# Performance work log

Hardware: AMD Instinct MI355X
Metric: run time of the kernel (lower is better)

The kernel has to match this reference:

```python
import jax, jax.numpy as jnp
import numpy as np

H = 8          # n_heads
DK = 128       # d_model // h
D = H * DK     # d_model = 1024
B, S = 8, 1024
D_LIST = (32, 64, 96, 128)  # sorted set of hidden//h from config dict


def setup_inputs() -> dict:
    key = jax.random.key(0)
    ks = jax.random.split(key, 13)
    mk = lambda k, shape: jax.random.normal(k, shape, dtype=jnp.float32)
    inp = {
        'query': mk(ks[0], (B, S, D)),
        'key': mk(ks[1], (B, S, D)),
        'value': mk(ks[2], (B, S, D)),
        'config_idx': jax.random.randint(ks[3], (B,), 0, len(D_LIST), dtype=jnp.int32),
        'Wq': mk(ks[4], (D, D)) * 0.02, 'bq': jnp.zeros((D,), jnp.float32),
        'Wk': mk(ks[5], (D, D)) * 0.02, 'bk': jnp.zeros((D,), jnp.float32),
        'Wv': mk(ks[6], (D, D)) * 0.02, 'bv': jnp.zeros((D,), jnp.float32),
        'Wo': mk(ks[7], (D, D)) * 0.02, 'bo': jnp.zeros((D,), jnp.float32),
    }
    return inp


def _mha_arrange(query, key, value, config_idx, Wq, bq, Wk, bk, Wv, bv, Wo, bo):
    Bb, Ss, _ = query.shape
    proj = lambda x, W, b: (x @ W.T + b).reshape(Bb, Ss, H, DK).transpose(0, 2, 1, 3)
    q = proj(query, Wq, bq)   # [B,H,S,DK]
    k = proj(key, Wk, bk)
    v = proj(value, Wv, bv)
    scores = jnp.einsum('bhqd,bhkd->bhqk', q, k) / np.float32(np.sqrt(DK))
    p = jax.nn.softmax(scores, axis=-1)
    ctx = jnp.einsum('bhqk,bhkd->bhqd', p, v).transpose(0, 2, 1, 3)  # [B,S,H,DK]
    # attn_arrange: per-sample width d; pack first d dims of each head densely
    ret = jnp.zeros((Bb, Ss, H * DK), query.dtype)
    for i, d in enumerate(D_LIST):
        packed = ctx[:, :, :, :d].reshape(Bb, Ss, H * d)           # [B,S,H*d]
        packed = jnp.pad(packed, ((0, 0), (0, 0), (0, H * (DK - d))))
        sel = (config_idx == i)[:, None, None]
        ret = ret + jnp.where(sel, packed, jnp.zeros((), query.dtype))
    return ret @ Wo.T + bo


def reference(query, key, value, config_idx, Wq, bq, Wk, bk, Wv, bv, Wo, bo):
    return _mha_arrange(query, key, value, config_idx, Wq, bq, Wk, bk, Wv, bv, Wo, bo)
```

## Files before the change

kernel.cpp:

```cpp
#include <hip/hip_runtime.h>
#include <hip/hip_bf16.h>


typedef __attribute__((ext_vector_type(8))) __bf16 bf16x8;
typedef __attribute__((ext_vector_type(4))) float f32x4;

#define DEV static __device__ __forceinline__

DEV float exp2v(float x) { return __builtin_amdgcn_exp2f(x); }

DEV unsigned short f2bf(float f) {
  union { float f; unsigned int u; } c; c.f = f;
  unsigned int u = c.u + 0x7fffu + ((c.u >> 16) & 1u);
  return (unsigned short)(u >> 16);
}

DEV unsigned cvtpk(float a, float b) {
  unsigned r;
  asm("v_cvt_pk_bf16_f32 %0, %1, %2" : "=v"(r) : "v"(a), "v"(b));
  return r;
}

DEV void gload16(const void* g, void* l) {
  __builtin_amdgcn_global_load_lds((const __attribute__((address_space(1))) void*)g,
                                   (__attribute__((address_space(3))) void*)l, 16, 0, 0);
}

#define LGKM0 do { asm volatile("s_waitcnt lgkmcnt(0)" ::: "memory"); \
                   __builtin_amdgcn_sched_barrier(0); } while (0)
#define BAR   __builtin_amdgcn_s_barrier()
#define VMC4  asm volatile("s_waitcnt vmcnt(4)" ::: "memory")
#define VMC0  asm volatile("s_waitcnt vmcnt(0)" ::: "memory")

DEV void cv4(const float* __restrict__ s, unsigned short* __restrict__ d, int i) {
  const float4 a = *(const float4*)(s + i);
  ushort4 o;
  o.x = f2bf(a.x); o.y = f2bf(a.y); o.z = f2bf(a.z); o.w = f2bf(a.w);
  *(ushort4*)(d + i) = o;
}

__global__ __launch_bounds__(256) void convert_kernel(
    const float* __restrict__ q, const float* __restrict__ k, const float* __restrict__ v,
    const float* __restrict__ wq, const float* __restrict__ wk,
    const float* __restrict__ wv, const float* __restrict__ wo,
    unsigned short* __restrict__ xq, unsigned short* __restrict__ xk,
    unsigned short* __restrict__ xv, unsigned short* __restrict__ wb)
{
  const int i = (blockIdx.x * 256 + threadIdx.x) * 4;
  cv4(q, xq, i);
  cv4(k, xk, i);
  cv4(v, xv, i);
  if (i < 4 * 1024 * 1024) {
    const int which = i >> 20, off = i & 1048575;
    const float* s = which == 0 ? wq : which == 1 ? wk : which == 2 ? wv : wo;
    cv4(s, wb + (which << 20), off);
  }
}

template<int OUTMODE>
__global__ __launch_bounds__(512, 2) void gemm8p(
    const unsigned short* __restrict__ xq, const unsigned short* __restrict__ xk,
    const unsigned short* __restrict__ xv, const unsigned short* __restrict__ wb,
    const float* __restrict__ bq, const float* __restrict__ bk,
    const float* __restrict__ bv,
    unsigned short* __restrict__ Qp, unsigned short* __restrict__ Kp,
    unsigned short* __restrict__ VTp, float* __restrict__ fout)
{
  __shared__ __align__(16) char LDS[131072];
  int z, mt, nt;
  if (OUTMODE == 0) {
    const int swz = ((blockIdx.x & 7) * 48) + (blockIdx.x >> 3);
    z = swz >> 7; const int rem = swz & 127; mt = rem >> 2; nt = rem & 3;
  } else {
    const int swz = ((blockIdx.x & 7) * 16) + (blockIdx.x >> 3);
    z = 0; mt = swz >> 2; nt = swz & 3;
  }
  const int m0 = mt * 256, n0 = nt * 256;
  const unsigned short* Ag = (OUTMODE == 1) ? xq : (z == 0 ? xq : z == 1 ? xk : xv);
  const unsigned short* Bg = (OUTMODE == 1) ? wb : wb + ((size_t)z << 20);
  const float* bias = (OUTMODE == 1) ? bq : (z == 0 ? bq : z == 1 ? bk : bv);

  const int tid = threadIdx.x, lane = tid & 63, w = tid >> 6;
  const int wm = w >> 2, wn = w & 3;
  const int g = lane >> 4, ln = lane & 15;

  const f32x4 fzero = {0.f, 0.f, 0.f, 0.f};
  f32x4 acc[8][4];
#pragma unroll
  for (int i = 0; i < 8; i++)
#pragma unroll
    for (int j = 0; j < 4; j++) acc[i][j] = fzero;

  bf16x8 bfr[4][2];
  bf16x8 afr[2][2];

  auto stageA = [&](int bf, int hf, int k0) {
    const unsigned short* src = Ag + (size_t)(m0 + hf * 128) * 1024 + k0;
    char* base = LDS + bf * 32768 + hf * 16384 + w * 2048;
#pragma unroll
    for (int r2 = 0; r2 < 2; ++r2) {
      const int o = w * 2048 + r2 * 1024 + lane * 16;
      const int rwi = o >> 7, cb = o & 127;
      gload16(src + (size_t)rwi * 1024 + ((cb ^ ((rwi & 7) << 4)) >> 1), base + r2 * 1024);
    }
  };
  auto stageB = [&](int bf, int hf, int k0) {
    const unsigned short* src = Bg + (size_t)(n0 + hf * 128) * 1024 + k0;
    char* base = LDS + 65536 + bf * 32768 + hf * 16384 + w * 2048;
#pragma unroll
    for (int r2 = 0; r2 < 2; ++r2) {
      const int o = w * 2048 + r2 * 1024 + lane * 16;
      const int rwi = o >> 7, cb = o & 127;
      gload16(src + (size_t)rwi * 1024 + ((cb ^ ((rwi & 7) << 4)) >> 1), base + r2 * 1024);
    }
  };
  auto rdA = [&](int bf, int q) {
#pragma unroll
    for (int p = 0; p < 2; ++p)
#pragma unroll
      for (int kc = 0; kc < 2; ++kc) {
        const int rwi = (2 * q + p) * 16 + ln;
        const int cb = (kc * 64 + g * 16) ^ ((rwi & 7) << 4);
        afr[p][kc] = *(const bf16x8*)(LDS + bf * 32768 + wm * 16384 + rwi * 128 + cb);
      }
  };
  auto rdB = [&](int bf) {
#pragma unroll
    for (int nf = 0; nf < 4; ++nf)
#pragma unroll
      for (int kc = 0; kc < 2; ++kc) {
        const int rwi = (wn & 1) * 64 + nf * 16 + ln;
        const int cb = (kc * 64 + g * 16) ^ ((rwi & 7) << 4);
        bfr[nf][kc] = *(const bf16x8*)(LDS + 65536 + bf * 32768 + (wn >> 1) * 16384 + rwi * 128 + cb);
      }
  };
  auto mm = [&](int q) {
    __builtin_amdgcn_s_setprio(1);
#pragma unroll
    for (int p = 0; p < 2; ++p)
#pragma unroll
      for (int nf = 0; nf < 4; ++nf)
#pragma unroll
        for (int kc = 0; kc < 2; ++kc)
          acc[2 * q + p][nf] =
              __builtin_amdgcn_mfma_f32_16x16x32_bf16(afr[p][kc], bfr[nf][kc],
                                                      acc[2 * q + p][nf], 0, 0, 0);
    __builtin_amdgcn_s_setprio(0);
  };

  stageB(0, 0, 0); stageB(0, 1, 0);
  stageA(0, 0, 0); stageA(0, 1, 0);
  stageB(1, 0, 64); stageB(1, 1, 64);
  VMC4; BAR;

  for (int j = 0; j < 8; ++j) {
    const int kO = (2 * j + 1) << 6, kNE = (2 * j + 2) << 6, kNO = (2 * j + 3) << 6;
    const bool pf = j < 7;
    rdB(0); rdA(0, 0); stageA(1, 0, kO);
    LGKM0; BAR; mm(0); BAR;
    rdA(0, 1); stageA(1, 1, kO);
    LGKM0; BAR; mm(1); BAR;
    rdA(0, 2); if (pf) stageB(0, 0, kNE);
    LGKM0; BAR; mm(2); BAR;
    rdA(0, 3); if (pf) stageB(0, 1, kNE);
    LGKM0; BAR; mm(3);
    if (pf) { VMC4; } else { VMC0; }
    BAR;
    rdB(1); rdA(1, 0); if (pf) stageA(0, 0, kNE);
    LGKM0; BAR; mm(0); BAR;
    rdA(1, 1); if (pf) stageA(0, 1, kNE);
    LGKM0; BAR; mm(1); BAR;
    rdA(1, 2); if (pf) stageB(1, 0, kNO);
    LGKM0; BAR; mm(2); BAR;
    rdA(1, 3); if (pf) stageB(1, 1, kNO);
    LGKM0; BAR; mm(3);
    if (pf) { VMC4; }
    BAR;
  }

  const float QS = 0.12751743f;
#pragma unroll
  for (int mf = 0; mf < 8; ++mf)
#pragma unroll
    for (int nf = 0; nf < 4; ++nf) {
      const int m = m0 + wm * 128 + mf * 16 + g * 4;
      const int n = n0 + wn * 64 + nf * 16 + ln;
      const float bn = bias[n];
      if (OUTMODE == 1) {
#pragma unroll
        for (int r = 0; r < 4; ++r)
          fout[(size_t)(m + r) * 1024 + n] = acc[mf][nf][r] + bn;
      } else if (z == 0) {
#pragma unroll
        for (int r = 0; r < 4; ++r)
          Qp[(size_t)(m + r) * 1024 + n] = f2bf((acc[mf][nf][r] + bn) * QS);
      } else if (z == 1) {
#pragma unroll
        for (int r = 0; r < 4; ++r)
          Kp[(size_t)(m + r) * 1024 + n] = f2bf(acc[mf][nf][r] + bn);
      } else {
        const int b = m >> 10, s0 = m & 1023;
        uint2 pk;
        pk.x = cvtpk(acc[mf][nf][0] + bn, acc[mf][nf][1] + bn);
        pk.y = cvtpk(acc[mf][nf][2] + bn, acc[mf][nf][3] + bn);
        *(uint2*)(VTp + (((size_t)(b * 8) << 7 | n) << 10) + s0) = pk;
      }
    }
}

__global__ __launch_bounds__(256) void attn_kernel(
    const unsigned short* __restrict__ Qp, const unsigned short* __restrict__ Kp,
    const unsigned short* __restrict__ VT, const int* __restrict__ cfg,
    unsigned short* __restrict__ ret)
{
  __shared__ __align__(16) unsigned short Ks[2][64 * 128];
  __shared__ __align__(16) unsigned short Vs[2][128 * 64];
  __shared__ __align__(16) unsigned short Ps[4 * 16 * 64];
  const int bx = blockIdx.x;
  const int qb = bx >> 6, bh = bx & 63, b = bh >> 3, h = bh & 7;
  const int tid = threadIdx.x, lane = tid & 63, w = tid >> 6;
  const int g = lane >> 4, ln = lane & 15;
  const int q0 = qb * 64;
  const f32x4 fzero = {0.f, 0.f, 0.f, 0.f};

  bf16x8 qf[4];
  {
    const unsigned short* qrow = Qp + ((size_t)(b * 1024 + q0 + w * 16 + ln)) * 1024 + h * 128;
#pragma unroll
    for (int kc = 0; kc < 4; kc++) qf[kc] = *(const bf16x8*)(qrow + kc * 32 + g * 8);
  }
  float m_run = -1e30f, l_run = 0.f;
  f32x4 o_acc[8];
#pragma unroll
  for (int i = 0; i < 8; i++) o_acc[i] = fzero;

  auto stage = [&](int buf, int kv0) {
#pragma unroll
    for (int i = 0; i < 4; ++i) {
      const int obase = i * 4096 + w * 1024;
      const int o = obase + lane * 16;
      {
        const int r = o >> 8, cb = o & 255;
        const int cs = cb ^ ((r & 7) << 4);
        gload16(Kp + ((size_t)(b * 1024 + kv0 + r)) * 1024 + h * 128 + (cs >> 1),
                (char*)Ks + buf * 16384 + obase);
      }
      {
        const int r = o >> 7, cb = o & 127;
        const int cs = cb ^ ((r & 7) << 4);
        gload16(VT + ((size_t)((b * 8 + h) * 128 + r)) * 1024 + kv0 + (cs >> 1),
                (char*)Vs + buf * 16384 + obase);
      }
    }
  };

  stage(0, 0);
  asm volatile("s_waitcnt vmcnt(0)" ::: "memory");
  __syncthreads();

  int cur = 0;
  for (int t = 0; t < 16; ++t) {
    if (t < 15) stage(cur ^ 1, (t + 1) * 64);

    f32x4 sc[4];
    __builtin_amdgcn_s_setprio(1);
#pragma unroll
    for (int nb = 0; nb < 4; ++nb) {
      sc[nb] = fzero;
      const int rr = nb * 16 + ln;
      const int sw = (rr & 7) << 4;
#pragma unroll
      for (int kc = 0; kc < 4; ++kc) {
        const bf16x8 kf = *(const bf16x8*)((const char*)Ks + cur * 16384 + rr * 256 +
                                           (((kc * 32 + g * 8) << 1) ^ sw));
        sc[nb] = __builtin_amdgcn_mfma_f32_16x16x32_bf16(kf, qf[kc], sc[nb], 0, 0, 0);
      }
    }
    __builtin_amdgcn_s_setprio(0);

    float mnb[4];
#pragma unroll
    for (int nb = 0; nb < 4; ++nb)
      mnb[nb] = fmaxf(fmaxf(sc[nb][0], sc[nb][1]), fmaxf(sc[nb][2], sc[nb][3]));
    float pmax = fmaxf(fmaxf(mnb[0], mnb[1]), fmaxf(mnb[2], mnb[3]));
    pmax = fmaxf(pmax, __shfl_xor(pmax, 16));
    pmax = fmaxf(pmax, __shfl_xor(pmax, 32));
    if (__any(pmax > m_run + 11.5f)) {
      const float mnew = fmaxf(m_run, pmax);
      const float alpha = exp2v(m_run - mnew);
      l_run *= alpha;
      m_run = mnew;
      float ar[4];
#pragma unroll
      for (int r = 0; r < 4; ++r)
        ar[r] = __shfl(alpha, (lane & 48) | (((lane >> 4) & 3) << 2) | r);
#pragma unroll
      for (int i = 0; i < 8; i++)
#pragma unroll
        for (int r = 0; r < 4; r++) o_acc[i][r] *= ar[r];
    }
    float sum = 0.f;
    float pvv[16];
#pragma unroll
    for (int nb = 0; nb < 4; ++nb)
#pragma unroll
      for (int r = 0; r < 4; ++r) {
        const float p = exp2v(sc[nb][r] - m_run);
        pvv[nb * 4 + r] = p; sum += p;
      }
    l_run += sum;

    {
      char* pbase = (char*)Ps + w * 2048 + ln * 128;
#pragma unroll
      for (int nb = 0; nb < 4; ++nb) {
        uint2 pk;
        pk.x = cvtpk(pvv[nb * 4 + 0], pvv[nb * 4 + 1]);
        pk.y = cvtpk(pvv[nb * 4 + 2], pvv[nb * 4 + 3]);
        *(uint2*)(pbase + (((16 * nb + 4 * g) << 1) ^ ((ln & 7) << 4))) = pk;
      }
    }
    bf16x8 pf[2];
#pragma unroll
    for (int kc = 0; kc < 2; kc++)
      pf[kc] = *(const bf16x8*)((const char*)Ps + w * 2048 + ln * 128 +
                                (((kc * 32 + g * 8) << 1) ^ ((ln & 7) << 4)));

    __builtin_amdgcn_s_setprio(1);
#pragma unroll
    for (int nb2 = 0; nb2 < 8; ++nb2) {
      const int rr = nb2 * 16 + ln;
      const int sw = (rr & 7) << 4;
#pragma unroll
      for (int kc = 0; kc < 2; ++kc) {
        const bf16x8 vf = *(const bf16x8*)((const char*)Vs + cur * 16384 + rr * 128 +
                                           (((kc * 32 + g * 8) << 1) ^ sw));
        o_acc[nb2] = __builtin_amdgcn_mfma_f32_16x16x32_bf16(pf[kc], vf, o_acc[nb2], 0, 0, 0);
      }
    }
    __builtin_amdgcn_s_setprio(0);

    if (t < 15) {
      asm volatile("s_waitcnt vmcnt(0)" ::: "memory");
      __syncthreads();
    }
    cur ^= 1;
  }

  l_run += __shfl_xor(l_run, 16);
  l_run += __shfl_xor(l_run, 32);
  float rl[4];
#pragma unroll
  for (int r = 0; r < 4; ++r)
    rl[r] = 1.0f / __shfl(l_run, (lane & 48) | (((lane >> 4) & 3) << 2) | r);
  const int d_b = 32 * (cfg[b] + 1);
  const int zw = 128 - d_b;
  const size_t rowbase = (size_t)(b * 1024 + q0 + w * 16 + g * 4);
#pragma unroll
  for (int nb2 = 0; nb2 < 8; ++nb2) {
    const int dk = nb2 * 16 + ln;
    if (dk < d_b) {
#pragma unroll
      for (int r = 0; r < 4; r++)
        ret[(rowbase + r) * 1024 + h * d_b + dk] = f2bf(o_acc[nb2][r] * rl[r]);
    } else {
#pragma unroll
      for (int r = 0; r < 4; r++)
        ret[(rowbase + r) * 1024 + 8 * d_b + h * zw + (dk - d_b)] = 0;
    }
  }
}

extern "C" void kernel_launch(void* const* d_in, const int* in_sizes, int n_in,
                              void* d_out, int out_size, void* d_ws, size_t ws_size,
                              hipStream_t stream)
{
  (void)in_sizes; (void)n_in; (void)out_size; (void)ws_size;
  const float* q   = (const float*)d_in[0];
  const float* k   = (const float*)d_in[1];
  const float* v   = (const float*)d_in[2];
  const int*   cfg = (const int*)d_in[3];
  const float* Wq  = (const float*)d_in[4];  const float* bq = (const float*)d_in[5];
  const float* Wk  = (const float*)d_in[6];  const float* bk = (const float*)d_in[7];
  const float* Wv  = (const float*)d_in[8];  const float* bv = (const float*)d_in[9];
  const float* Wo  = (const float*)d_in[10]; const float* bo = (const float*)d_in[11];

  const size_t X  = 8192ull * 1024ull;
  const size_t WN = 1024ull * 1024ull;
  char* p = (char*)d_ws;
  unsigned short* xq  = (unsigned short*)p; p += X * 2;
  unsigned short* xk  = (unsigned short*)p; p += X * 2;
  unsigned short* xv  = (unsigned short*)p; p += X * 2;
  unsigned short* wb  = (unsigned short*)p; p += 4 * WN * 2;
  unsigned short* Qp  = (unsigned short*)p; p += X * 2;
  unsigned short* Kp  = (unsigned short*)p; p += X * 2;
  unsigned short* VTp = (unsigned short*)p; p += X * 2;
  unsigned short* ret = (unsigned short*)p; p += X * 2;

  convert_kernel<<<dim3(8192), dim3(256), 0, stream>>>(q, k, v, Wq, Wk, Wv, Wo,
                                                       xq, xk, xv, wb);

  gemm8p<0><<<dim3(384), dim3(512), 0, stream>>>(xq, xk, xv, wb, bq, bk, bv,
                                                 Qp, Kp, VTp, nullptr);

  attn_kernel<<<dim3(1024), dim3(256), 0, stream>>>(Qp, Kp, VTp, cfg, ret);

  gemm8p<1><<<dim3(128), dim3(512), 0, stream>>>(ret, nullptr, nullptr, wb + 3 * WN,
                                                 bo, nullptr, nullptr,
                                                 nullptr, nullptr, nullptr,
                                                 (float*)d_out);
}
```

Before: 194.7 us.

## Shrink GEMM tiles to 256x128 with triple buffering and enlarge attention blocks

The projection GEMMs move from 256x256 tiles to 256x128 tiles, which doubles the grid so more CUs are busy. They also switch to a three-stage LDS ring buffer with one barrier pair per K step and drop the sched_barrier in the LDS wait. The attention kernel now uses 512 threads handling 128 query rows per block, halving the grid and sharing each K/V stage across twice as many queries. The risks are higher LDS use (144KB per GEMM block, occupancy 1), more B-operand reloads with the smaller N tile, and possible scheduling problems once the sched barrier is gone.

After: 171.5 us. 1.14x faster.

```diff
diff --git a/kernel.cpp b/kernel.cpp
--- a/kernel.cpp
+++ b/kernel.cpp
@@ -26,10 +26,9 @@
                                    (__attribute__((address_space(3))) void*)l, 16, 0, 0);
 }
 
-#define LGKM0 do { asm volatile("s_waitcnt lgkmcnt(0)" ::: "memory"); \
-                   __builtin_amdgcn_sched_barrier(0); } while (0)
+#define LGKM0 asm volatile("s_waitcnt lgkmcnt(0)" ::: "memory")
 #define BAR   __builtin_amdgcn_s_barrier()
-#define VMC4  asm volatile("s_waitcnt vmcnt(4)" ::: "memory")
+#define VMC6  asm volatile("s_waitcnt vmcnt(6)" ::: "memory")
 #define VMC0  asm volatile("s_waitcnt vmcnt(0)" ::: "memory")
 
 DEV void cv4(const float* __restrict__ s, unsigned short* __restrict__ d, int i) {
@@ -58,7 +57,7 @@
 }
 
 template<int OUTMODE>
-__global__ __launch_bounds__(512, 2) void gemm8p(
+__global__ __launch_bounds__(512, 1) void gemmS(
     const unsigned short* __restrict__ xq, const unsigned short* __restrict__ xk,
     const unsigned short* __restrict__ xv, const unsigned short* __restrict__ wb,
     const float* __restrict__ bq, const float* __restrict__ bk,
@@ -66,35 +65,35 @@
     unsigned short* __restrict__ Qp, unsigned short* __restrict__ Kp,
     unsigned short* __restrict__ VTp, float* __restrict__ fout)
 {
-  __shared__ __align__(16) char LDS[131072];
+  __shared__ __align__(16) char LDS[147456];
   int z, mt, nt;
   if (OUTMODE == 0) {
-    const int swz = ((blockIdx.x & 7) * 48) + (blockIdx.x >> 3);
-    z = swz >> 7; const int rem = swz & 127; mt = rem >> 2; nt = rem & 3;
+    const int swz = (blockIdx.x & 7) * 96 + (blockIdx.x >> 3);
+    z = swz >> 8; const int rem = swz & 255; mt = rem >> 3; nt = rem & 7;
   } else {
-    const int swz = ((blockIdx.x & 7) * 16) + (blockIdx.x >> 3);
-    z = 0; mt = swz >> 2; nt = swz & 3;
-  }
-  const int m0 = mt * 256, n0 = nt * 256;
+    const int swz = (blockIdx.x & 7) * 32 + (blockIdx.x >> 3);
+    z = 0; mt = swz >> 3; nt = swz & 7;
+  }
+  const int m0 = mt * 256, n0 = nt * 128;
   const unsigned short* Ag = (OUTMODE == 1) ? xq : (z == 0 ? xq : z == 1 ? xk : xv);
   const unsigned short* Bg = (OUTMODE == 1) ? wb : wb + ((size_t)z << 20);
   const float* bias = (OUTMODE == 1) ? bq : (z == 0 ? bq : z == 1 ? bk : bv);
 
   const int tid = threadIdx.x, lane = tid & 63, w = tid >> 6;
-  const int wm = w >> 2, wn = w & 3;
+  const int wm = w >> 1, wn = w & 1;
   const int g = lane >> 4, ln = lane & 15;
 
   const f32x4 fzero = {0.f, 0.f, 0.f, 0.f};
-  f32x4 acc[8][4];
-#pragma unroll
-  for (int i = 0; i < 8; i++)
+  f32x4 acc[4][4];
+#pragma unroll
+  for (int i = 0; i < 4; i++)
 #pragma unroll
     for (int j = 0; j < 4; j++) acc[i][j] = fzero;
 
   bf16x8 bfr[4][2];
   bf16x8 afr[2][2];
 
-  auto stageA = [&](int bf, int hf, int k0) {
+  auto SA = [&](int bf, int hf, int k0) {
     const unsigned short* src = Ag + (size_t)(m0 + hf * 128) * 1024 + k0;
     char* base = LDS + bf * 32768 + hf * 16384 + w * 2048;
 #pragma unroll
@@ -104,9 +103,9 @@
       gload16(src + (size_t)rwi * 1024 + ((cb ^ ((rwi & 7) << 4)) >> 1), base + r2 * 1024);
     }
   };
-  auto stageB = [&](int bf, int hf, int k0) {
-    const unsigned short* src = Bg + (size_t)(n0 + hf * 128) * 1024 + k0;
-    char* base = LDS + 65536 + bf * 32768 + hf * 16384 + w * 2048;
+  auto SB = [&](int bf, int k0) {
+    const unsigned short* src = Bg + (size_t)n0 * 1024 + k0;
+    char* base = LDS + 98304 + bf * 16384 + w * 2048;
 #pragma unroll
     for (int r2 = 0; r2 < 2; ++r2) {
       const int o = w * 2048 + r2 * 1024 + lane * 16;
@@ -116,23 +115,23 @@
   };
   auto rdA = [&](int bf, int q) {
 #pragma unroll
-    for (int p = 0; p < 2; ++p)
-#pragma unroll
-      for (int kc = 0; kc < 2; ++kc) {
-        const int rwi = (2 * q + p) * 16 + ln;
-        const int cb = (kc * 64 + g * 16) ^ ((rwi & 7) << 4);
-        afr[p][kc] = *(const bf16x8*)(LDS + bf * 32768 + wm * 16384 + rwi * 128 + cb);
-      }
+    for (int p = 0; p < 2; ++p) {
+      const int row = wm * 64 + (2 * q + p) * 16 + ln;
+      const int sw = (row & 7) << 4;
+#pragma unroll
+      for (int kc = 0; kc < 2; ++kc)
+        afr[p][kc] = *(const bf16x8*)(LDS + bf * 32768 + row * 128 + ((kc * 64 + g * 16) ^ sw));
+    }
   };
   auto rdB = [&](int bf) {
 #pragma unroll
-    for (int nf = 0; nf < 4; ++nf)
-#pragma unroll
-      for (int kc = 0; kc < 2; ++kc) {
-        const int rwi = (wn & 1) * 64 + nf * 16 + ln;
-        const int cb = (kc * 64 + g * 16) ^ ((rwi & 7) << 4);
-        bfr[nf][kc] = *(const bf16x8*)(LDS + 65536 + bf * 32768 + (wn >> 1) * 16384 + rwi * 128 + cb);
-      }
+    for (int nf = 0; nf < 4; ++nf) {
+      const int row = wn * 64 + nf * 16 + ln;
+      const int sw = (row & 7) << 4;
+#pragma unroll
+      for (int kc = 0; kc < 2; ++kc)
+        bfr[nf][kc] = *(const bf16x8*)(LDS + 98304 + bf * 16384 + row * 128 + ((kc * 64 + g * 16) ^ sw));
+    }
   };
   auto mm = [&](int q) {
     __builtin_amdgcn_s_setprio(1);
@@ -148,42 +147,31 @@
     __builtin_amdgcn_s_setprio(0);
   };
 
-  stageB(0, 0, 0); stageB(0, 1, 0);
-  stageA(0, 0, 0); stageA(0, 1, 0);
-  stageB(1, 0, 64); stageB(1, 1, 64);
-  VMC4; BAR;
-
-  for (int j = 0; j < 8; ++j) {
-    const int kO = (2 * j + 1) << 6, kNE = (2 * j + 2) << 6, kNO = (2 * j + 3) << 6;
-    const bool pf = j < 7;
-    rdB(0); rdA(0, 0); stageA(1, 0, kO);
-    LGKM0; BAR; mm(0); BAR;
-    rdA(0, 1); stageA(1, 1, kO);
-    LGKM0; BAR; mm(1); BAR;
-    rdA(0, 2); if (pf) stageB(0, 0, kNE);
-    LGKM0; BAR; mm(2); BAR;
-    rdA(0, 3); if (pf) stageB(0, 1, kNE);
-    LGKM0; BAR; mm(3);
-    if (pf) { VMC4; } else { VMC0; }
+  SA(0, 0, 0); SA(0, 1, 0); SB(0, 0);
+  SA(1, 0, 64); SA(1, 1, 64); SB(1, 64);
+  VMC6; BAR;
+
+  int br = 0, bw = 2;
+  for (int t = 0; t < 16; ++t) {
+    const int kL = (t + 2) << 6;
+    rdB(br); rdA(br, 0);
+    if (t < 14) { SA(bw, 0, kL); SA(bw, 1, kL); }
+    BAR; LGKM0; mm(0); BAR;
+    rdA(br, 1);
+    if (t < 14) SB(bw, kL);
+    BAR; LGKM0; mm(1);
+    if (t < 14) { VMC6; } else if (t == 14) { VMC0; }
     BAR;
-    rdB(1); rdA(1, 0); if (pf) stageA(0, 0, kNE);
-    LGKM0; BAR; mm(0); BAR;
-    rdA(1, 1); if (pf) stageA(0, 1, kNE);
-    LGKM0; BAR; mm(1); BAR;
-    rdA(1, 2); if (pf) stageB(1, 0, kNO);
-    LGKM0; BAR; mm(2); BAR;
-    rdA(1, 3); if (pf) stageB(1, 1, kNO);
-    LGKM0; BAR; mm(3);
-    if (pf) { VMC4; }
-    BAR;
+    br = br == 2 ? 0 : br + 1;
+    bw = bw == 2 ? 0 : bw + 1;
   }
 
   const float QS = 0.12751743f;
 #pragma unroll
-  for (int mf = 0; mf < 8; ++mf)
+  for (int mf = 0; mf < 4; ++mf)
 #pragma unroll
     for (int nf = 0; nf < 4; ++nf) {
-      const int m = m0 + wm * 128 + mf * 16 + g * 4;
+      const int m = m0 + wm * 64 + mf * 16 + g * 4;
       const int n = n0 + wn * 64 + nf * 16 + ln;
       const float bn = bias[n];
       if (OUTMODE == 1) {
@@ -203,24 +191,24 @@
         uint2 pk;
         pk.x = cvtpk(acc[mf][nf][0] + bn, acc[mf][nf][1] + bn);
         pk.y = cvtpk(acc[mf][nf][2] + bn, acc[mf][nf][3] + bn);
-        *(uint2*)(VTp + (((size_t)(b * 8) << 7 | n) << 10) + s0) = pk;
-      }
-    }
-}
-
-__global__ __launch_bounds__(256) void attn_kernel(
+        *(uint2*)(VTp + (((size_t)(b * 1024 + n)) << 10) + s0) = pk;
+      }
+    }
+}
+
+__global__ __launch_bounds__(512) void attn_kernel(
     const unsigned short* __restrict__ Qp, const unsigned short* __restrict__ Kp,
     const unsigned short* __restrict__ VT, const int* __restrict__ cfg,
     unsigned short* __restrict__ ret)
 {
   __shared__ __align__(16) unsigned short Ks[2][64 * 128];
   __shared__ __align__(16) unsigned short Vs[2][128 * 64];
-  __shared__ __align__(16) unsigned short Ps[4 * 16 * 64];
+  __shared__ __align__(16) unsigned short Ps[8 * 16 * 64];
   const int bx = blockIdx.x;
   const int qb = bx >> 6, bh = bx & 63, b = bh >> 3, h = bh & 7;
   const int tid = threadIdx.x, lane = tid & 63, w = tid >> 6;
   const int g = lane >> 4, ln = lane & 15;
-  const int q0 = qb * 64;
+  const int q0 = qb * 128;
   const f32x4 fzero = {0.f, 0.f, 0.f, 0.f};
 
   bf16x8 qf[4];
@@ -236,20 +224,19 @@
 
   auto stage = [&](int buf, int kv0) {
 #pragma unroll
-    for (int i = 0; i < 4; ++i) {
-      const int obase = i * 4096 + w * 1024;
-      const int o = obase + lane * 16;
+    for (int i = 0; i < 2; ++i) {
+      const int o = i * 8192 + tid * 16;
       {
         const int r = o >> 8, cb = o & 255;
         const int cs = cb ^ ((r & 7) << 4);
         gload16(Kp + ((size_t)(b * 1024 + kv0 + r)) * 1024 + h * 128 + (cs >> 1),
-                (char*)Ks + buf * 16384 + obase);
+                (char*)Ks + buf * 16384 + o);
       }
       {
         const int r = o >> 7, cb = o & 127;
         const int cs = cb ^ ((r & 7) << 4);
         gload16(VT + ((size_t)((b * 8 + h) * 128 + r)) * 1024 + kv0 + (cs >> 1),
-                (char*)Vs + buf * 16384 + obase);
+                (char*)Vs + buf * 16384 + o);
       }
     }
   };
@@ -400,13 +387,13 @@
   convert_kernel<<<dim3(8192), dim3(256), 0, stream>>>(q, k, v, Wq, Wk, Wv, Wo,
                                                        xq, xk, xv, wb);
 
-  gemm8p<0><<<dim3(384), dim3(512), 0, stream>>>(xq, xk, xv, wb, bq, bk, bv,
-                                                 Qp, Kp, VTp, nullptr);
-
-  attn_kernel<<<dim3(1024), dim3(256), 0, stream>>>(Qp, Kp, VTp, cfg, ret);
-
-  gemm8p<1><<<dim3(128), dim3(512), 0, stream>>>(ret, nullptr, nullptr, wb + 3 * WN,
-                                                 bo, nullptr, nullptr,
-                                                 nullptr, nullptr, nullptr,
-                                                 (float*)d_out);
-}
+  gemmS<0><<<dim3(768), dim3(512), 0, stream>>>(xq, xk, xv, wb, bq, bk, bv,
+                                                Qp, Kp, VTp, nullptr);
+
+  attn_kernel<<<dim3(512), dim3(512), 0, stream>>>(Qp, Kp, VTp, cfg, ret);
+
+  gemmS<1><<<dim3(256), dim3(512), 0, stream>>>(ret, nullptr, nullptr, wb + 3 * WN,
+                                                bo, nullptr, nullptr,
+                                                nullptr, nullptr, nullptr,
+                                                (float*)d_out);
+}
```
